# Kernel optimization log

Hardware: AMD Instinct MI355X
Metric: run time of the kernel (lower is better)

The kernel has to match this reference:

```python
import jax, jax.numpy as jnp
import numpy as np

WINDOW = 11
K1, K2, L, EPS = 0.01, 0.03, 1.0, 1e-8


def _box_filter(x, window):
    # Depthwise normalized box filter, VALID padding. x: (B, C, H, W)
    c = x.shape[1]
    k = jnp.ones((c, 1, window, window), dtype=x.dtype) / (window * window)
    return jax.lax.conv_general_dilated(
        x, k, window_strides=(1, 1), padding='VALID',
        dimension_numbers=('NCHW', 'OIHW', 'NCHW'),
        feature_group_count=c)


def setup_inputs() -> dict:
    key = jax.random.key(0)
    kx, ky = jax.random.split(key)
    shape = (16, 3, 512, 512)
    x = jax.random.uniform(kx, shape, dtype=jnp.float32)
    y = jax.random.uniform(ky, shape, dtype=jnp.float32)
    return {"x": x, "y": y}


def reference(x, y):
    C1 = (K1 * L) ** 2
    C2 = (K2 * L) ** 2
    mu_x = _box_filter(x, WINDOW)
    mu_y = _box_filter(y, WINDOW)
    mu_x_sq = mu_x * mu_x
    mu_y_sq = mu_y * mu_y
    mu_xy = mu_x * mu_y
    sigma_x_sq = jnp.maximum(_box_filter(x * x, WINDOW) - mu_x_sq, 0.0)
    sigma_y_sq = jnp.maximum(_box_filter(y * y, WINDOW) - mu_y_sq, 0.0)
    sigma_xy = _box_filter(x * y, WINDOW) - mu_xy
    num = (2.0 * mu_xy + C1) * (2.0 * sigma_xy + C2)
    den = (mu_x_sq + mu_y_sq + C1) * (sigma_x_sq + sigma_y_sq + C2) + EPS
    ssim = jnp.mean(num / den)
    return 1.0 - ssim
```

## Files before the change

kernel.cpp:

```cpp
#include <hip/hip_runtime.h>


#define WIN     11
#define IMG     512
#define PLSZ    (IMG * IMG)
#define OUTW    502
#define SEG     8
#define NSEG    63
#define NPLANES 48
#define NPART   (NSEG * NPLANES)

#define C1S   1.4641f
#define C2S   13.1769f
#define EPS4  2.1434881f

__global__ __launch_bounds__(64) void ssim_zero(double* acc) {
    if (threadIdx.x == 0) acc[0] = 0.0;
}

__global__ __launch_bounds__(64) void ssim_main(const float* __restrict__ x,
                                                const float* __restrict__ y,
                                                double* __restrict__ part,
                                                int mode) {
    __shared__ __align__(16) float H[5][2][264];

    const int lane  = threadIdx.x;
    const int seg   = blockIdx.x;
    const int plane = blockIdx.y;
    const int o0    = seg * SEG;
    const int o1    = (o0 + SEG < OUTW) ? (o0 + SEG) : OUTW;
    const int r0    = o0;
    const int r1    = o1 + WIN - 2;
    const int c0    = 8 * lane;

    if (lane < 20) {
        const int q = lane >> 2, rem = lane & 3;
        *(float4*)&H[q][rem >> 1][256 + ((rem & 1) << 2)] =
            make_float4(0.f, 0.f, 0.f, 0.f);
    }

    const float* xp = x + plane * PLSZ;
    const float* yp = y + plane * PLSZ;

    float Vx[8]  = {0,0,0,0,0,0,0,0};
    float Vy[8]  = {0,0,0,0,0,0,0,0};
    float Vxx[8] = {0,0,0,0,0,0,0,0};
    float Vyy[8] = {0,0,0,0,0,0,0,0};
    float Vxy[8] = {0,0,0,0,0,0,0,0};

    const float4 z4 = make_float4(0.f, 0.f, 0.f, 0.f);
    float4 nx0, nx1, ny0, ny1;
    float4 nX0 = z4, nX1 = z4, nY0 = z4, nY1 = z4;
    float4 ox0 = z4, ox1 = z4, oy0 = z4, oy1 = z4;
    float4 oX0 = z4, oX1 = z4, oY0 = z4, oY1 = z4;

    {
        const float4* px = (const float4*)(xp + r0 * IMG + c0);
        const float4* py = (const float4*)(yp + r0 * IMG + c0);
        nx0 = px[0]; nx1 = px[1]; ny0 = py[0]; ny1 = py[1];
    }

    float lsum = 0.f;

    for (int r = r0; r <= r1; ++r) {
        const int rn = r + 1;
        if (rn <= r1) {
            const float4* px = (const float4*)(xp + rn * IMG + c0);
            const float4* py = (const float4*)(yp + rn * IMG + c0);
            nX0 = px[0]; nX1 = px[1]; nY0 = py[0]; nY1 = py[1];
            const int ro = rn - WIN;
            if (ro >= r0) {
                const float4* qx = (const float4*)(xp + ro * IMG + c0);
                const float4* qy = (const float4*)(yp + ro * IMG + c0);
                oX0 = qx[0]; oX1 = qx[1]; oY0 = qy[0]; oY1 = qy[1];
            }
        }

        {
            const float xn[8] = {nx0.x,nx0.y,nx0.z,nx0.w, nx1.x,nx1.y,nx1.z,nx1.w};
            const float yn[8] = {ny0.x,ny0.y,ny0.z,ny0.w, ny1.x,ny1.y,ny1.z,ny1.w};
#pragma unroll
            for (int j = 0; j < 8; ++j) {
                Vx[j] += xn[j];
                Vy[j] += yn[j];
                Vxx[j] = fmaf(xn[j], xn[j], Vxx[j]);
                Vyy[j] = fmaf(yn[j], yn[j], Vyy[j]);
                Vxy[j] = fmaf(xn[j], yn[j], Vxy[j]);
            }
        }
        if (r - r0 >= WIN) {
            const float xo[8] = {ox0.x,ox0.y,ox0.z,ox0.w, ox1.x,ox1.y,ox1.z,ox1.w};
            const float yo[8] = {oy0.x,oy0.y,oy0.z,oy0.w, oy1.x,oy1.y,oy1.z,oy1.w};
#pragma unroll
            for (int j = 0; j < 8; ++j) {
                Vx[j] -= xo[j];
                Vy[j] -= yo[j];
                Vxx[j] = fmaf(-xo[j], xo[j], Vxx[j]);
                Vyy[j] = fmaf(-yo[j], yo[j], Vyy[j]);
                Vxy[j] = fmaf(-xo[j], yo[j], Vxy[j]);
            }
        }

        if (r - r0 >= WIN - 1) {
            __builtin_amdgcn_wave_barrier();
            ((float4*)&H[0][0][4 * lane])[0] = make_float4(Vx[0],  Vx[1],  Vx[2],  Vx[3]);
            ((float4*)&H[0][1][4 * lane])[0] = make_float4(Vx[4],  Vx[5],  Vx[6],  Vx[7]);
            ((float4*)&H[1][0][4 * lane])[0] = make_float4(Vy[0],  Vy[1],  Vy[2],  Vy[3]);
            ((float4*)&H[1][1][4 * lane])[0] = make_float4(Vy[4],  Vy[5],  Vy[6],  Vy[7]);
            ((float4*)&H[2][0][4 * lane])[0] = make_float4(Vxx[0], Vxx[1], Vxx[2], Vxx[3]);
            ((float4*)&H[2][1][4 * lane])[0] = make_float4(Vxx[4], Vxx[5], Vxx[6], Vxx[7]);
            ((float4*)&H[3][0][4 * lane])[0] = make_float4(Vyy[0], Vyy[1], Vyy[2], Vyy[3]);
            ((float4*)&H[3][1][4 * lane])[0] = make_float4(Vyy[4], Vyy[5], Vyy[6], Vyy[7]);
            ((float4*)&H[4][0][4 * lane])[0] = make_float4(Vxy[0], Vxy[1], Vxy[2], Vxy[3]);
            ((float4*)&H[4][1][4 * lane])[0] = make_float4(Vxy[4], Vxy[5], Vxy[6], Vxy[7]);
            __builtin_amdgcn_wave_barrier();

            float h[5][8];
#define HORIZ(Q, VA)                                                           \
            {                                                                  \
                const float4 lo1 = *(const float4*)&H[Q][0][4 * lane + 4];     \
                const float4 hi1 = *(const float4*)&H[Q][1][4 * lane + 4];     \
                const float4 lo2 = *(const float4*)&H[Q][0][4 * lane + 8];     \
                float s = ((VA[0] + VA[1]) + (VA[2] + VA[3]))                  \
                        + ((VA[4] + VA[5]) + (VA[6] + VA[7]));                 \
                s += (lo1.x + lo1.y) + lo1.z;                                  \
                h[Q][0] = s;                                                   \
                s += lo1.w - VA[0]; h[Q][1] = s;                               \
                s += hi1.x - VA[1]; h[Q][2] = s;                               \
                s += hi1.y - VA[2]; h[Q][3] = s;                               \
                s += hi1.z - VA[3]; h[Q][4] = s;                               \
                s += hi1.w - VA[4]; h[Q][5] = s;                               \
                s += lo2.x - VA[5]; h[Q][6] = s;                               \
                s += lo2.y - VA[6]; h[Q][7] = s;                               \
            }
            HORIZ(0, Vx)
            HORIZ(1, Vy)
            HORIZ(2, Vxx)
            HORIZ(3, Vyy)
            HORIZ(4, Vxy)
#undef HORIZ

#pragma unroll
            for (int j = 0; j < 8; ++j) {
                if (c0 + j < OUTW) {
                    const float X  = h[0][j], Y  = h[1][j];
                    const float XX = h[2][j], YY = h[3][j], XY = h[4][j];
                    const float x2 = X * X, y2 = Y * Y, xy = X * Y;
                    const float A  = fmaf(2.f, xy, C1S);
                    const float B  = fmaf(2.f, fmaf(121.f, XY, -xy), C2S);
                    const float Cc = x2 + y2 + C1S;
                    const float sx = fmaxf(fmaf(121.f, XX, -x2), 0.f);
                    const float sy = fmaxf(fmaf(121.f, YY, -y2), 0.f);
                    const float D  = (sx + sy) + C2S;
                    const float den = fmaf(Cc, D, EPS4);
                    float rr = __builtin_amdgcn_rcpf(den);
                    rr = rr * (2.f - den * rr);
                    lsum = fmaf(A * B, rr, lsum);
                }
            }
        }

        nx0 = nX0; nx1 = nX1; ny0 = nY0; ny1 = nY1;
        ox0 = oX0; ox1 = oX1; oy0 = oY0; oy1 = oY1;
    }

#pragma unroll
    for (int off = 32; off > 0; off >>= 1) lsum += __shfl_down(lsum, off, 64);
    if (lane == 0) {
        if (mode == 0) part[plane * NSEG + seg] = (double)lsum;
        else           atomicAdd(part, (double)lsum);
    }
}

__global__ __launch_bounds__(256) void ssim_final(const double* __restrict__ part,
                                                  int n, float* __restrict__ out) {
    __shared__ double s[4];
    double v = 0.0;
    for (int i = threadIdx.x; i < n; i += 256) v += part[i];
#pragma unroll
    for (int off = 32; off > 0; off >>= 1) v += __shfl_down(v, off, 64);
    if ((threadIdx.x & 63) == 0) s[threadIdx.x >> 6] = v;
    __syncthreads();
    if (threadIdx.x == 0) {
        double tot = (s[0] + s[1]) + (s[2] + s[3]);
        const double N = (double)NPLANES * OUTW * OUTW;
        out[0] = 1.0f - (float)(tot / N);
    }
}

extern "C" void kernel_launch(void* const* d_in, const int* in_sizes, int n_in,
                              void* d_out, int out_size, void* d_ws, size_t ws_size,
                              hipStream_t stream) {
    const float* x = (const float*)d_in[0];
    const float* y = (const float*)d_in[1];
    float* out = (float*)d_out;
    double* part = (double*)d_ws;

    if (ws_size >= (size_t)NPART * sizeof(double)) {
        ssim_main<<<dim3(NSEG, NPLANES), dim3(64), 0, stream>>>(x, y, part, 0);
        ssim_final<<<dim3(1), dim3(256), 0, stream>>>(part, NPART, out);
    } else {
        ssim_zero<<<dim3(1), dim3(64), 0, stream>>>(part);
        ssim_main<<<dim3(NSEG, NPLANES), dim3(64), 0, stream>>>(x, y, part, 1);
        ssim_final<<<dim3(1), dim3(256), 0, stream>>>(part, 1, out);
    }
}
```

Before: 150.0 us.

## Replace LDS horizontal pass with register halo loads and remap block schedule

Measured after the change: 142.3 us. 5.1% less time.

```diff
diff --git a/kernel.cpp b/kernel.cpp
--- a/kernel.cpp
+++ b/kernel.cpp
@@ -5,10 +5,10 @@
 #define IMG     512
 #define PLSZ    (IMG * IMG)
 #define OUTW    502
-#define SEG     8
-#define NSEG    63
+#define SEG     12
+#define NSEG    42
 #define NPLANES 48
-#define NPART   (NSEG * NPLANES)
+#define NBLK    (NSEG * NPLANES)
 
 #define C1S   1.4641f
 #define C2S   13.1769f
@@ -18,69 +18,85 @@
     if (threadIdx.x == 0) acc[0] = 0.0;
 }
 
-__global__ __launch_bounds__(64) void ssim_main(const float* __restrict__ x,
-                                                const float* __restrict__ y,
-                                                double* __restrict__ part,
-                                                int mode) {
-    __shared__ __align__(16) float H[5][2][264];
-
-    const int lane  = threadIdx.x;
-    const int seg   = blockIdx.x;
-    const int plane = blockIdx.y;
-    const int o0    = seg * SEG;
-    const int o1    = (o0 + SEG < OUTW) ? (o0 + SEG) : OUTW;
-    const int r0    = o0;
-    const int r1    = o1 + WIN - 2;
-    const int c0    = 8 * lane;
-
-    if (lane < 20) {
-        const int q = lane >> 2, rem = lane & 3;
-        *(float4*)&H[q][rem >> 1][256 + ((rem & 1) << 2)] =
-            make_float4(0.f, 0.f, 0.f, 0.f);
-    }
+__global__ __launch_bounds__(64, 2) void ssim_main(const float* __restrict__ x,
+                                                   const float* __restrict__ y,
+                                                   double* __restrict__ part,
+                                                   int mode) {
+    const int lane = threadIdx.x;
+    const int id   = blockIdx.x;
+    const int q8    = id >> 3;
+    const int plane = (id & 7) + 8 * (q8 / NSEG);
+    const int seg   = q8 % NSEG;
+
+    const int o0 = seg * SEG;
+    const int o1 = (o0 + SEG < OUTW) ? (o0 + SEG) : OUTW;
+    const int r0 = o0;
+    const int r1 = o1 + WIN - 2;
+
+    const int c0 = 8 * lane;
+    const int a0 = c0;
+    const int a1 = c0 + 4;
+    const int a2 = (c0 + 8  < 508) ? (c0 + 8)  : 508;
+    const int a3 = (c0 + 12 < 508) ? (c0 + 12) : 508;
+    const int a4 = (c0 + 16 < 510) ? (c0 + 16) : 510;
 
     const float* xp = x + plane * PLSZ;
     const float* yp = y + plane * PLSZ;
 
-    float Vx[8]  = {0,0,0,0,0,0,0,0};
-    float Vy[8]  = {0,0,0,0,0,0,0,0};
-    float Vxx[8] = {0,0,0,0,0,0,0,0};
-    float Vyy[8] = {0,0,0,0,0,0,0,0};
-    float Vxy[8] = {0,0,0,0,0,0,0,0};
+#define LOADROW(P, R, v0, v1, v2, v3, v4)                        \
+    { const float* rp_ = (P) + ((R) << 9);                       \
+      v0 = *(const float4*)(rp_ + a0);                           \
+      v1 = *(const float4*)(rp_ + a1);                           \
+      v2 = *(const float4*)(rp_ + a2);                           \
+      v3 = *(const float4*)(rp_ + a3);                           \
+      v4 = *(const float2*)(rp_ + a4); }
+
+#define UNPACK(v0, v1, v2, v3, v4, arr)                          \
+    { arr[0]=v0.x;  arr[1]=v0.y;  arr[2]=v0.z;  arr[3]=v0.w;     \
+      arr[4]=v1.x;  arr[5]=v1.y;  arr[6]=v1.z;  arr[7]=v1.w;     \
+      arr[8]=v2.x;  arr[9]=v2.y;  arr[10]=v2.z; arr[11]=v2.w;    \
+      arr[12]=v3.x; arr[13]=v3.y; arr[14]=v3.z; arr[15]=v3.w;    \
+      arr[16]=v4.x; arr[17]=v4.y; }
+
+    float Vx[18], Vy[18], Vxx[18], Vyy[18], Vxy[18];
+#pragma unroll
+    for (int j = 0; j < 18; ++j) {
+        Vx[j] = 0.f; Vy[j] = 0.f; Vxx[j] = 0.f; Vyy[j] = 0.f; Vxy[j] = 0.f;
+    }
 
     const float4 z4 = make_float4(0.f, 0.f, 0.f, 0.f);
-    float4 nx0, nx1, ny0, ny1;
-    float4 nX0 = z4, nX1 = z4, nY0 = z4, nY1 = z4;
-    float4 ox0 = z4, ox1 = z4, oy0 = z4, oy1 = z4;
-    float4 oX0 = z4, oX1 = z4, oY0 = z4, oY1 = z4;
-
-    {
-        const float4* px = (const float4*)(xp + r0 * IMG + c0);
-        const float4* py = (const float4*)(yp + r0 * IMG + c0);
-        nx0 = px[0]; nx1 = px[1]; ny0 = py[0]; ny1 = py[1];
-    }
+    const float2 z2 = make_float2(0.f, 0.f);
+    float4 cnx0, cnx1, cnx2, cnx3; float2 cnx4;
+    float4 cny0, cny1, cny2, cny3; float2 cny4;
+    float4 cox0 = z4, cox1 = z4, cox2 = z4, cox3 = z4; float2 cox4 = z2;
+    float4 coy0 = z4, coy1 = z4, coy2 = z4, coy3 = z4; float2 coy4 = z2;
+    float4 nnx0 = z4, nnx1 = z4, nnx2 = z4, nnx3 = z4; float2 nnx4 = z2;
+    float4 nny0 = z4, nny1 = z4, nny2 = z4, nny3 = z4; float2 nny4 = z2;
+    float4 nox0 = z4, nox1 = z4, nox2 = z4, nox3 = z4; float2 nox4 = z2;
+    float4 noy0 = z4, noy1 = z4, noy2 = z4, noy3 = z4; float2 noy4 = z2;
+
+    LOADROW(xp, r0, cnx0, cnx1, cnx2, cnx3, cnx4)
+    LOADROW(yp, r0, cny0, cny1, cny2, cny3, cny4)
 
     float lsum = 0.f;
 
     for (int r = r0; r <= r1; ++r) {
-        const int rn = r + 1;
-        if (rn <= r1) {
-            const float4* px = (const float4*)(xp + rn * IMG + c0);
-            const float4* py = (const float4*)(yp + rn * IMG + c0);
-            nX0 = px[0]; nX1 = px[1]; nY0 = py[0]; nY1 = py[1];
-            const int ro = rn - WIN;
-            if (ro >= r0) {
-                const float4* qx = (const float4*)(xp + ro * IMG + c0);
-                const float4* qy = (const float4*)(yp + ro * IMG + c0);
-                oX0 = qx[0]; oX1 = qx[1]; oY0 = qy[0]; oY1 = qy[1];
-            }
+        if (r < r1) {
+            LOADROW(xp, r + 1, nnx0, nnx1, nnx2, nnx3, nnx4)
+            LOADROW(yp, r + 1, nny0, nny1, nny2, nny3, nny4)
+        }
+        const int ro = r + 1 - WIN;
+        if (ro >= r0) {
+            LOADROW(xp, ro, nox0, nox1, nox2, nox3, nox4)
+            LOADROW(yp, ro, noy0, noy1, noy2, noy3, noy4)
         }
 
         {
-            const float xn[8] = {nx0.x,nx0.y,nx0.z,nx0.w, nx1.x,nx1.y,nx1.z,nx1.w};
-            const float yn[8] = {ny0.x,ny0.y,ny0.z,ny0.w, ny1.x,ny1.y,ny1.z,ny1.w};
-#pragma unroll
-            for (int j = 0; j < 8; ++j) {
+            float xn[18], yn[18];
+            UNPACK(cnx0, cnx1, cnx2, cnx3, cnx4, xn)
+            UNPACK(cny0, cny1, cny2, cny3, cny4, yn)
+#pragma unroll
+            for (int j = 0; j < 18; ++j) {
                 Vx[j] += xn[j];
                 Vy[j] += yn[j];
                 Vxx[j] = fmaf(xn[j], xn[j], Vxx[j]);
@@ -89,10 +105,11 @@
             }
         }
         if (r - r0 >= WIN) {
-            const float xo[8] = {ox0.x,ox0.y,ox0.z,ox0.w, ox1.x,ox1.y,ox1.z,ox1.w};
-            const float yo[8] = {oy0.x,oy0.y,oy0.z,oy0.w, oy1.x,oy1.y,oy1.z,oy1.w};
-#pragma unroll
-            for (int j = 0; j < 8; ++j) {
+            float xo[18], yo[18];
+            UNPACK(cox0, cox1, cox2, cox3, cox4, xo)
+            UNPACK(coy0, coy1, coy2, coy3, coy4, yo)
+#pragma unroll
+            for (int j = 0; j < 18; ++j) {
                 Vx[j] -= xo[j];
                 Vy[j] -= yo[j];
                 Vxx[j] = fmaf(-xo[j], xo[j], Vxx[j]);
@@ -102,72 +119,54 @@
         }
 
         if (r - r0 >= WIN - 1) {
-            __builtin_amdgcn_wave_barrier();
-            ((float4*)&H[0][0][4 * lane])[0] = make_float4(Vx[0],  Vx[1],  Vx[2],  Vx[3]);
-            ((float4*)&H[0][1][4 * lane])[0] = make_float4(Vx[4],  Vx[5],  Vx[6],  Vx[7]);
-            ((float4*)&H[1][0][4 * lane])[0] = make_float4(Vy[0],  Vy[1],  Vy[2],  Vy[3]);
-            ((float4*)&H[1][1][4 * lane])[0] = make_float4(Vy[4],  Vy[5],  Vy[6],  Vy[7]);
-            ((float4*)&H[2][0][4 * lane])[0] = make_float4(Vxx[0], Vxx[1], Vxx[2], Vxx[3]);
-            ((float4*)&H[2][1][4 * lane])[0] = make_float4(Vxx[4], Vxx[5], Vxx[6], Vxx[7]);
-            ((float4*)&H[3][0][4 * lane])[0] = make_float4(Vyy[0], Vyy[1], Vyy[2], Vyy[3]);
-            ((float4*)&H[3][1][4 * lane])[0] = make_float4(Vyy[4], Vyy[5], Vyy[6], Vyy[7]);
-            ((float4*)&H[4][0][4 * lane])[0] = make_float4(Vxy[0], Vxy[1], Vxy[2], Vxy[3]);
-            ((float4*)&H[4][1][4 * lane])[0] = make_float4(Vxy[4], Vxy[5], Vxy[6], Vxy[7]);
-            __builtin_amdgcn_wave_barrier();
-
-            float h[5][8];
-#define HORIZ(Q, VA)                                                           \
-            {                                                                  \
-                const float4 lo1 = *(const float4*)&H[Q][0][4 * lane + 4];     \
-                const float4 hi1 = *(const float4*)&H[Q][1][4 * lane + 4];     \
-                const float4 lo2 = *(const float4*)&H[Q][0][4 * lane + 8];     \
-                float s = ((VA[0] + VA[1]) + (VA[2] + VA[3]))                  \
-                        + ((VA[4] + VA[5]) + (VA[6] + VA[7]));                 \
-                s += (lo1.x + lo1.y) + lo1.z;                                  \
-                h[Q][0] = s;                                                   \
-                s += lo1.w - VA[0]; h[Q][1] = s;                               \
-                s += hi1.x - VA[1]; h[Q][2] = s;                               \
-                s += hi1.y - VA[2]; h[Q][3] = s;                               \
-                s += hi1.z - VA[3]; h[Q][4] = s;                               \
-                s += hi1.w - VA[4]; h[Q][5] = s;                               \
-                s += lo2.x - VA[5]; h[Q][6] = s;                               \
-                s += lo2.y - VA[6]; h[Q][7] = s;                               \
-            }
-            HORIZ(0, Vx)
-            HORIZ(1, Vy)
-            HORIZ(2, Vxx)
-            HORIZ(3, Vyy)
-            HORIZ(4, Vxy)
-#undef HORIZ
-
+#define SUM11(V, s)                                                       \
+            { float t0_ = V[0] + V[1], t1_ = V[2] + V[3];                 \
+              float t2_ = V[4] + V[5], t3_ = V[6] + V[7];                 \
+              float t4_ = V[8] + V[9];                                    \
+              s = ((t0_ + t1_) + (t2_ + t3_)) + (t4_ + V[10]); }
+            float s0, s1, s2, s3, s4;
+            SUM11(Vx,  s0)
+            SUM11(Vy,  s1)
+            SUM11(Vxx, s2)
+            SUM11(Vyy, s3)
+            SUM11(Vxy, s4)
+#undef SUM11
 #pragma unroll
             for (int j = 0; j < 8; ++j) {
-                if (c0 + j < OUTW) {
-                    const float X  = h[0][j], Y  = h[1][j];
-                    const float XX = h[2][j], YY = h[3][j], XY = h[4][j];
-                    const float x2 = X * X, y2 = Y * Y, xy = X * Y;
-                    const float A  = fmaf(2.f, xy, C1S);
-                    const float B  = fmaf(2.f, fmaf(121.f, XY, -xy), C2S);
-                    const float Cc = x2 + y2 + C1S;
-                    const float sx = fmaxf(fmaf(121.f, XX, -x2), 0.f);
-                    const float sy = fmaxf(fmaf(121.f, YY, -y2), 0.f);
-                    const float D  = (sx + sy) + C2S;
-                    const float den = fmaf(Cc, D, EPS4);
-                    float rr = __builtin_amdgcn_rcpf(den);
-                    rr = rr * (2.f - den * rr);
-                    lsum = fmaf(A * B, rr, lsum);
+                const float X = s0, Y = s1, XX = s2, YY = s3, XY = s4;
+                const float x2 = X * X, y2 = Y * Y, xy = X * Y;
+                const float A  = fmaf(2.f, xy, C1S);
+                const float B  = fmaf(2.f, fmaf(121.f, XY, -xy), C2S);
+                const float Cc = (x2 + y2) + C1S;
+                const float sx = fmaxf(fmaf(121.f, XX, -x2), 0.f);
+                const float sy = fmaxf(fmaf(121.f, YY, -y2), 0.f);
+                const float D  = (sx + sy) + C2S;
+                const float den = fmaf(Cc, D, EPS4);
+                float rr = __builtin_amdgcn_rcpf(den);
+                rr = rr * (2.f - den * rr);
+                if (c0 + j < OUTW) lsum = fmaf(A * B, rr, lsum);
+                if (j < 7) {
+                    s0 += Vx[j + 11]  - Vx[j];
+                    s1 += Vy[j + 11]  - Vy[j];
+                    s2 += Vxx[j + 11] - Vxx[j];
+                    s3 += Vyy[j + 11] - Vyy[j];
+                    s4 += Vxy[j + 11] - Vxy[j];
                 }
             }
         }
 
-        nx0 = nX0; nx1 = nX1; ny0 = nY0; ny1 = nY1;
-        ox0 = oX0; ox1 = oX1; oy0 = oY0; oy1 = oY1;
-    }
+        cnx0 = nnx0; cnx1 = nnx1; cnx2 = nnx2; cnx3 = nnx3; cnx4 = nnx4;
+        cny0 = nny0; cny1 = nny1; cny2 = nny2; cny3 = nny3; cny4 = nny4;
+        cox0 = nox0; cox1 = nox1; cox2 = nox2; cox3 = nox3; cox4 = nox4;
+        coy0 = noy0; coy1 = noy1; coy2 = noy2; coy3 = noy3; coy4 = noy4;
+    }
+#undef LOADROW
+#undef UNPACK
 
 #pragma unroll
     for (int off = 32; off > 0; off >>= 1) lsum += __shfl_down(lsum, off, 64);
     if (lane == 0) {
-        if (mode == 0) part[plane * NSEG + seg] = (double)lsum;
+        if (mode == 0) part[id] = (double)lsum;
         else           atomicAdd(part, (double)lsum);
     }
 }
@@ -196,12 +195,12 @@
     float* out = (float*)d_out;
     double* part = (double*)d_ws;
 
-    if (ws_size >= (size_t)NPART * sizeof(double)) {
-        ssim_main<<<dim3(NSEG, NPLANES), dim3(64), 0, stream>>>(x, y, part, 0);
-        ssim_final<<<dim3(1), dim3(256), 0, stream>>>(part, NPART, out);
+    if (ws_size >= (size_t)NBLK * sizeof(double)) {
+        ssim_main<<<dim3(NBLK), dim3(64), 0, stream>>>(x, y, part, 0);
+        ssim_final<<<dim3(1), dim3(256), 0, stream>>>(part, NBLK, out);
     } else {
         ssim_zero<<<dim3(1), dim3(64), 0, stream>>>(part);
-        ssim_main<<<dim3(NSEG, NPLANES), dim3(64), 0, stream>>>(x, y, part, 1);
+        ssim_main<<<dim3(NBLK), dim3(64), 0, stream>>>(x, y, part, 1);
         ssim_final<<<dim3(1), dim3(256), 0, stream>>>(part, 1, out);
     }
 }
```
